# Kernel tuning notes

Measured on AMD Instinct MI355X. Metric: run time of the kernel, lower is better.

The kernel has to match this reference:

```python
import jax, jax.numpy as jnp
import numpy as np

N_NODES = 50000
N_EDGES = 1200000
H = 64
N_CONV = 3
N_GRAPHS = 64
N_CLASSES = 10


def rbf_cutoff(d):
    # Gaussian radial basis over (0,1) with cosine cutoff, per edge -> [E, H]
    mu = jnp.linspace(0.0, 1.0, H, dtype=d.dtype)
    gamma = jnp.asarray(float(H), d.dtype)  # inverse width
    bf = jnp.exp(-gamma * (d[:, None] - mu[None, :]) ** 2)
    cut = 0.5 * (jnp.cos(jnp.pi * jnp.clip(d, 0.0, 1.0)) + 1.0)
    return bf * cut[:, None]


def mlp(x, W1, b1, W2, b2):
    # Linear -> softplus -> Linear (SchNet-style filter/embedding MLP)
    return jax.nn.softplus(x @ W1 + b1) @ W2 + b2


def setup_inputs() -> dict:
    key = jax.random.key(0)
    ks = jax.random.split(key, 12)
    s = 0.1  # weight scale for numerical stability
    inp = {
        "d": jax.random.uniform(ks[0], (N_EDGES,), jnp.float32),
        "W_emb1": s * jax.random.normal(ks[1], (H, H), jnp.float32),
        "b_emb1": jnp.zeros((H,), jnp.float32),
        "W_emb2": s * jax.random.normal(ks[2], (H, H), jnp.float32),
        "b_emb2": jnp.zeros((H,), jnp.float32),
        "filt_W1": s * jax.random.normal(ks[3], (N_CONV, H, H), jnp.float32),
        "filt_b1": jnp.zeros((N_CONV, H), jnp.float32),
        "filt_W2": s * jax.random.normal(ks[4], (N_CONV, H, H), jnp.float32),
        "filt_b2": jnp.zeros((N_CONV, H), jnp.float32),
        "W_in": s * jax.random.normal(ks[5], (N_CONV, H, H), jnp.float32),
        "b_in": jnp.zeros((N_CONV, H), jnp.float32),
        "W_out": s * jax.random.normal(ks[6], (N_CONV, H, H), jnp.float32),
        "b_out": jnp.zeros((N_CONV, H), jnp.float32),
        "W_fc": s * jax.random.normal(ks[7], (H, N_CLASSES), jnp.float32),
        "b_fc": jnp.zeros((N_CLASSES,), jnp.float32),
        "src": jax.random.randint(ks[8], (N_EDGES,), 0, N_NODES, jnp.int32),
        "dst": jax.random.randint(ks[9], (N_EDGES,), 0, N_NODES, jnp.int32),
        "node_graph_ids": jnp.sort(jax.random.randint(ks[10], (N_NODES,), 0, N_GRAPHS, jnp.int32)),
    }
    return inp


def reference(d, W_emb1, b_emb1, W_emb2, b_emb2,
              filt_W1, filt_b1, filt_W2, filt_b2,
              W_in, b_in, W_out, b_out, W_fc, b_fc,
              src, dst, node_graph_ids):
    bf = rbf_cutoff(d)  # [E, H], basis * cutoff (g.edata['bf'])

    # SchnetEmbedding: MLP over radial features, scatter-add to destination nodes
    x = jax.ops.segment_sum(mlp(bf, W_emb1, b_emb1, W_emb2, b_emb2),
                            dst, num_segments=N_NODES)  # [N, H]

    # Stacked SchnetConv: gather x[src] -> in-proj -> radial filter modulation -> scatter-add -> out-proj
    for l in range(N_CONV):
        filt = mlp(bf, filt_W1[l], filt_b1[l], filt_W2[l], filt_b2[l])  # [E, H]
        m = (x[src] @ W_in[l] + b_in[l]) * filt                          # [E, H]
        agg = jax.ops.segment_sum(m, dst, num_segments=N_NODES)         # [N, H]
        x = jax.nn.relu(agg @ W_out[l] + b_out[l])

    # dgl.mean_nodes: per-graph mean pooling
    counts = jax.ops.segment_sum(jnp.ones((N_NODES,), x.dtype),
                                 node_graph_ids, num_segments=N_GRAPHS)
    pooled = jax.ops.segment_sum(x, node_graph_ids, num_segments=N_GRAPHS)
    pooled = pooled / jnp.maximum(counts, 1.0)[:, None]  # [B, H]

    logits = pooled @ W_fc + b_fc
    return jax.nn.log_softmax(logits, axis=1)
```

## Files before the change

kernel.cpp:

```cpp
#include <hip/hip_runtime.h>
#include <math.h>

#define H 64
#define NCONV 3
#define NGRAPHS 64
#define NCLASSES 10
#define TBL 8192
#define TROWS (TBL + 1)

typedef unsigned short bfu;

__device__ __forceinline__ float bf2f(bfu u) {
    return __uint_as_float(((unsigned int)u) << 16);
}
__device__ __forceinline__ bfu f2bf(float f) {
    unsigned int x = __float_as_uint(f);
    return (bfu)((x + 0x7FFF + ((x >> 16) & 1)) >> 16);
}
__device__ __forceinline__ float softplus_f(float x) {
    return fmaxf(x, 0.f) + log1pf(expf(-fabsf(x)));
}
__device__ __forceinline__ float bflo(unsigned int u) { return __uint_as_float(u << 16); }
__device__ __forceinline__ float bfhi(unsigned int u) { return __uint_as_float(u & 0xFFFF0000u); }

__device__ __forceinline__ unsigned int ld_rec_nt(const unsigned int* p) {
    return __builtin_nontemporal_load(p);
}
#define REC_SRC(u) ((u) & 0x1FFFFu)
#define REC_T(u)   ((u) >> 17)

__global__ void build_tables(const float* __restrict__ W_emb1, const float* __restrict__ b_emb1,
                             const float* __restrict__ W_emb2, const float* __restrict__ b_emb2,
                             const float* __restrict__ fW1, const float* __restrict__ fb1,
                             const float* __restrict__ fW2, const float* __restrict__ fb2,
                             bfu* __restrict__ tabs)
{
    int which = blockIdx.y;
    const float *W1, *b1, *W2, *b2;
    if (which == 0) { W1 = W_emb1; b1 = b_emb1; W2 = W_emb2; b2 = b_emb2; }
    else {
        int l = which - 1;
        W1 = fW1 + l * H * H; b1 = fb1 + l * H;
        W2 = fW2 + l * H * H; b2 = fb2 + l * H;
    }

    __shared__ float sW1[H * H], sW2[H * H];
    __shared__ float sb1[H], sb2[H];
    __shared__ float sha[4][H], shb[4][H];

    int tid = threadIdx.x;
    for (int i = tid; i < H * H; i += 256) { sW1[i] = W1[i]; sW2[i] = W2[i]; }
    if (tid < H) sb1[tid] = b1[tid];
    else if (tid < 2 * H) sb2[tid - H] = b2[tid - H];
    __syncthreads();

    int wave = tid >> 6, lane = tid & 63;
    int base = blockIdx.x * 64;
    int lim  = min(base + 64, TROWS);

    for (int r = base + wave; r < lim; r += 4) {
        float dv   = (float)r / (float)TBL;
        float mu   = (float)lane / (float)(H - 1);
        float diff = dv - mu;
        float cut  = 0.5f * (cosf(3.14159265358979323846f * dv) + 1.0f);
        float bfj  = expf(-(float)H * diff * diff) * cut;

        sha[wave][lane] = bfj;
        float a = sb1[lane];
        #pragma unroll
        for (int i = 0; i < H; ++i) a = fmaf(sha[wave][i], sW1[i * H + lane], a);
        shb[wave][lane] = softplus_f(a);
        float a2 = sb2[lane];
        #pragma unroll
        for (int i = 0; i < H; ++i) a2 = fmaf(shb[wave][i], sW2[i * H + lane], a2);

        tabs[((size_t)which * TROWS + r) * H + lane] = f2bf(a2);
    }
}

__global__ void hist_rank(const int* __restrict__ dst, int* __restrict__ cnt,
                          int* __restrict__ rank, int E) {
    int e = blockIdx.x * blockDim.x + threadIdx.x;
    if (e < E) rank[e] = atomicAdd(&cnt[dst[e]], 1);
}

__global__ void scan_bsum(const int* __restrict__ cnt, int* __restrict__ bsum, int N) {
    __shared__ int s[256];
    int t = threadIdx.x;
    int i = blockIdx.x * 256 + t;
    s[t] = (i < N) ? cnt[i] : 0;
    __syncthreads();
    for (int o = 128; o > 0; o >>= 1) {
        if (t < o) s[t] += s[t + o];
        __syncthreads();
    }
    if (t == 0) bsum[blockIdx.x] = s[0];
}

__global__ void scan_gsum(const int* __restrict__ bsum, int* __restrict__ gsum, int nblk) {
    __shared__ int s[1024];
    int t = threadIdx.x;
    s[t] = (t < nblk) ? bsum[t] : 0;
    __syncthreads();
    for (int o = 1; o < 1024; o <<= 1) {
        int v = (t >= o) ? s[t - o] : 0;
        __syncthreads();
        s[t] += v;
        __syncthreads();
    }
    if (t < nblk) gsum[t] = s[t] - bsum[t];
}

__global__ void scan_off(const int* __restrict__ cnt, const int* __restrict__ gsum,
                         int* __restrict__ off, int N) {
    __shared__ int s[256];
    int t = threadIdx.x;
    int i = blockIdx.x * 256 + t;
    int v = (i < N) ? cnt[i] : 0;
    s[t] = v;
    __syncthreads();
    for (int o = 1; o < 256; o <<= 1) {
        int u = (t >= o) ? s[t - o] : 0;
        __syncthreads();
        s[t] += u;
        __syncthreads();
    }
    int incl = s[t] + gsum[blockIdx.x];
    if (i < N) {
        off[i] = incl - v;
        if (i == N - 1) off[N] = incl;
    }
}

__global__ void scatter_kernel(const int* __restrict__ src, const int* __restrict__ dst,
                               const float* __restrict__ d, const int* __restrict__ off,
                               const int* __restrict__ rank, unsigned int* __restrict__ recs, int E)
{
    int e = blockIdx.x * blockDim.x + threadIdx.x;
    if (e >= E) return;
    int pos = off[dst[e]] + rank[e];
    float dv = fminf(fmaxf(d[e], 0.f), 1.f);
    int t = (int)(dv * (float)TBL + 0.5f);
    t = min(t, TBL);
    recs[pos] = (unsigned int)src[e] | ((unsigned int)t << 17);
}

__global__ void emb_fused(const int* __restrict__ off, const unsigned int* __restrict__ recs,
                          const bfu* __restrict__ tab, const float* __restrict__ W,
                          const float* __restrict__ bvec, bfu* __restrict__ yout, int N)
{
    __shared__ float sW[H * H];
    __shared__ float sb[H];
    __shared__ float sx[4][H];
    int tid = threadIdx.x;
    for (int i = tid; i < H * H; i += 256) sW[i] = W[i];
    if (tid < H) sb[tid] = bvec[tid];
    __syncthreads();

    const unsigned int* tab32 = (const unsigned int*)tab;

    int wave = tid >> 6, lane = tid & 63;
    int half = lane >> 5;
    int li   = lane & 31;

    for (int k = 0; k < 4; ++k) {
        int node = blockIdx.x * 16 + k * 4 + wave;
        if (node >= N) continue;
        int b = off[node], en = off[node + 1];
        int deg = en - b;
        int c0  = (deg + 1) >> 1;
        int p   = b + half * c0;
        int e   = (half == 0) ? (b + c0) : en;

        float a0 = 0.f, a1 = 0.f, a2 = 0.f, a3 = 0.f;

        if (e - p >= 8) {
            unsigned int u0 = ld_rec_nt(recs + p);
            unsigned int u1 = ld_rec_nt(recs + p + 1);
            unsigned int u2 = ld_rec_nt(recs + p + 2);
            unsigned int u3 = ld_rec_nt(recs + p + 3);
            unsigned int tv0 = tab32[(size_t)REC_T(u0) * 32 + li];
            unsigned int tv1 = tab32[(size_t)REC_T(u1) * 32 + li];
            unsigned int tv2 = tab32[(size_t)REC_T(u2) * 32 + li];
            unsigned int tv3 = tab32[(size_t)REC_T(u3) * 32 + li];
            u0 = ld_rec_nt(recs + p + 4);
            u1 = ld_rec_nt(recs + p + 5);
            u2 = ld_rec_nt(recs + p + 6);
            u3 = ld_rec_nt(recs + p + 7);
            while (p + 12 <= e) {
                unsigned int w0 = ld_rec_nt(recs + p + 8);
                unsigned int w1 = ld_rec_nt(recs + p + 9);
                unsigned int w2 = ld_rec_nt(recs + p + 10);
                unsigned int w3 = ld_rec_nt(recs + p + 11);
                unsigned int n0 = tab32[(size_t)REC_T(u0) * 32 + li];
                unsigned int n1 = tab32[(size_t)REC_T(u1) * 32 + li];
                unsigned int n2 = tab32[(size_t)REC_T(u2) * 32 + li];
                unsigned int n3 = tab32[(size_t)REC_T(u3) * 32 + li];
                a0 += bflo(tv0); a1 += bfhi(tv0);
                a2 += bflo(tv1); a3 += bfhi(tv1);
                a0 += bflo(tv2); a1 += bfhi(tv2);
                a2 += bflo(tv3); a3 += bfhi(tv3);
                tv0 = n0; tv1 = n1; tv2 = n2; tv3 = n3;
                u0 = w0; u1 = w1; u2 = w2; u3 = w3;
                p += 4;
            }
            unsigned int n0 = tab32[(size_t)REC_T(u0) * 32 + li];
            unsigned int n1 = tab32[(size_t)REC_T(u1) * 32 + li];
            unsigned int n2 = tab32[(size_t)REC_T(u2) * 32 + li];
            unsigned int n3 = tab32[(size_t)REC_T(u3) * 32 + li];
            a0 += bflo(tv0); a1 += bfhi(tv0);
            a2 += bflo(tv1); a3 += bfhi(tv1);
            a0 += bflo(tv2); a1 += bfhi(tv2);
            a2 += bflo(tv3); a3 += bfhi(tv3);
            a0 += bflo(n0); a1 += bfhi(n0);
            a2 += bflo(n1); a3 += bfhi(n1);
            a0 += bflo(n2); a1 += bfhi(n2);
            a2 += bflo(n3); a3 += bfhi(n3);
            p += 8;
        } else if (e - p >= 4) {
            unsigned int u0 = ld_rec_nt(recs + p);
            unsigned int u1 = ld_rec_nt(recs + p + 1);
            unsigned int u2 = ld_rec_nt(recs + p + 2);
            unsigned int u3 = ld_rec_nt(recs + p + 3);
            unsigned int n0 = tab32[(size_t)REC_T(u0) * 32 + li];
            unsigned int n1 = tab32[(size_t)REC_T(u1) * 32 + li];
            unsigned int n2 = tab32[(size_t)REC_T(u2) * 32 + li];
            unsigned int n3 = tab32[(size_t)REC_T(u3) * 32 + li];
            a0 += bflo(n0); a1 += bfhi(n0);
            a2 += bflo(n1); a3 += bfhi(n1);
            a0 += bflo(n2); a1 += bfhi(n2);
            a2 += bflo(n3); a3 += bfhi(n3);
            p += 4;
        }
        for (; p < e; ++p) {
            unsigned int u = ld_rec_nt(recs + p);
            unsigned int t = tab32[(size_t)REC_T(u) * 32 + li];
            a0 += bflo(t); a1 += bfhi(t);
        }

        float alo = a0 + a2, ahi = a1 + a3;
        alo += __shfl_down(alo, 32);
        ahi += __shfl_down(ahi, 32);
        if (lane < 32) {
            sx[wave][2 * li]     = alo;
            sx[wave][2 * li + 1] = ahi;
        }
        float o = sb[lane];
        #pragma unroll
        for (int i = 0; i < H; ++i) o = fmaf(sx[wave][i], sW[i * H + lane], o);
        yout[(size_t)node * H + lane] = f2bf(o);
    }
}

template <bool LAST>
__global__ void conv_fused_k(const int* __restrict__ off, const unsigned int* __restrict__ recs,
                             const bfu* __restrict__ tab, const bfu* __restrict__ y,
                             const float* __restrict__ W_out, const float* __restrict__ b_out,
                             bfu* __restrict__ yout, float* __restrict__ xout, int N)
{
    __shared__ float sW[H * H];
    __shared__ float sb[H];
    __shared__ float sx[4][H];
    int tid = threadIdx.x;
    for (int i = tid; i < H * H; i += 256) sW[i] = W_out[i];
    if (tid < H) sb[tid] = b_out[tid];
    __syncthreads();

    const unsigned int* tab32 = (const unsigned int*)tab;
    const unsigned int* y32   = (const unsigned int*)y;

    int wave = tid >> 6, lane = tid & 63;
    int half = lane >> 5;
    int li   = lane & 31;

    for (int k = 0; k < 4; ++k) {
        int node = blockIdx.x * 16 + k * 4 + wave;
        if (node >= N) continue;
        int b = off[node], en = off[node + 1];
        int deg = en - b;
        int c0  = (deg + 1) >> 1;
        int p   = b + half * c0;
        int e   = (half == 0) ? (b + c0) : en;

        float a0 = 0.f, a1 = 0.f, a2 = 0.f, a3 = 0.f;

        if (e - p >= 8) {
            unsigned int u0 = ld_rec_nt(recs + p);
            unsigned int u1 = ld_rec_nt(recs + p + 1);
            unsigned int u2 = ld_rec_nt(recs + p + 2);
            unsigned int u3 = ld_rec_nt(recs + p + 3);
            unsigned int tv0 = tab32[(size_t)REC_T(u0) * 32 + li];
            unsigned int yv0 = y32[(size_t)REC_SRC(u0) * 32 + li];
            unsigned int tv1 = tab32[(size_t)REC_T(u1) * 32 + li];
            unsigned int yv1 = y32[(size_t)REC_SRC(u1) * 32 + li];
            unsigned int tv2 = tab32[(size_t)REC_T(u2) * 32 + li];
            unsigned int yv2 = y32[(size_t)REC_SRC(u2) * 32 + li];
            unsigned int tv3 = tab32[(size_t)REC_T(u3) * 32 + li];
            unsigned int yv3 = y32[(size_t)REC_SRC(u3) * 32 + li];
            u0 = ld_rec_nt(recs + p + 4);
            u1 = ld_rec_nt(recs + p + 5);
            u2 = ld_rec_nt(recs + p + 6);
            u3 = ld_rec_nt(recs + p + 7);
            while (p + 12 <= e) {
                unsigned int w0 = ld_rec_nt(recs + p + 8);
                unsigned int w1 = ld_rec_nt(recs + p + 9);
                unsigned int w2 = ld_rec_nt(recs + p + 10);
                unsigned int w3 = ld_rec_nt(recs + p + 11);
                unsigned int nt0 = tab32[(size_t)REC_T(u0) * 32 + li];
                unsigned int ny0 = y32[(size_t)REC_SRC(u0) * 32 + li];
                unsigned int nt1 = tab32[(size_t)REC_T(u1) * 32 + li];
                unsigned int ny1 = y32[(size_t)REC_SRC(u1) * 32 + li];
                unsigned int nt2 = tab32[(size_t)REC_T(u2) * 32 + li];
                unsigned int ny2 = y32[(size_t)REC_SRC(u2) * 32 + li];
                unsigned int nt3 = tab32[(size_t)REC_T(u3) * 32 + li];
                unsigned int ny3 = y32[(size_t)REC_SRC(u3) * 32 + li];
                a0 = fmaf(bflo(yv0), bflo(tv0), a0);
                a1 = fmaf(bfhi(yv0), bfhi(tv0), a1);
                a2 = fmaf(bflo(yv1), bflo(tv1), a2);
                a3 = fmaf(bfhi(yv1), bfhi(tv1), a3);
                a0 = fmaf(bflo(yv2), bflo(tv2), a0);
                a1 = fmaf(bfhi(yv2), bfhi(tv2), a1);
                a2 = fmaf(bflo(yv3), bflo(tv3), a2);
                a3 = fmaf(bfhi(yv3), bfhi(tv3), a3);
                tv0 = nt0; yv0 = ny0; tv1 = nt1; yv1 = ny1;
                tv2 = nt2; yv2 = ny2; tv3 = nt3; yv3 = ny3;
                u0 = w0; u1 = w1; u2 = w2; u3 = w3;
                p += 4;
            }
            unsigned int nt0 = tab32[(size_t)REC_T(u0) * 32 + li];
            unsigned int ny0 = y32[(size_t)REC_SRC(u0) * 32 + li];
            unsigned int nt1 = tab32[(size_t)REC_T(u1) * 32 + li];
            unsigned int ny1 = y32[(size_t)REC_SRC(u1) * 32 + li];
            unsigned int nt2 = tab32[(size_t)REC_T(u2) * 32 + li];
            unsigned int ny2 = y32[(size_t)REC_SRC(u2) * 32 + li];
            unsigned int nt3 = tab32[(size_t)REC_T(u3) * 32 + li];
            unsigned int ny3 = y32[(size_t)REC_SRC(u3) * 32 + li];
            a0 = fmaf(bflo(yv0), bflo(tv0), a0);
            a1 = fmaf(bfhi(yv0), bfhi(tv0), a1);
            a2 = fmaf(bflo(yv1), bflo(tv1), a2);
            a3 = fmaf(bfhi(yv1), bfhi(tv1), a3);
            a0 = fmaf(bflo(yv2), bflo(tv2), a0);
            a1 = fmaf(bfhi(yv2), bfhi(tv2), a1);
            a2 = fmaf(bflo(yv3), bflo(tv3), a2);
            a3 = fmaf(bfhi(yv3), bfhi(tv3), a3);
            a0 = fmaf(bflo(ny0), bflo(nt0), a0);
            a1 = fmaf(bfhi(ny0), bfhi(nt0), a1);
            a2 = fmaf(bflo(ny1), bflo(nt1), a2);
            a3 = fmaf(bfhi(ny1), bfhi(nt1), a3);
            a0 = fmaf(bflo(ny2), bflo(nt2), a0);
            a1 = fmaf(bfhi(ny2), bfhi(nt2), a1);
            a2 = fmaf(bflo(ny3), bflo(nt3), a2);
            a3 = fmaf(bfhi(ny3), bfhi(nt3), a3);
            p += 8;
        } else if (e - p >= 4) {
            unsigned int u0 = ld_rec_nt(recs + p);
            unsigned int u1 = ld_rec_nt(recs + p + 1);
            unsigned int u2 = ld_rec_nt(recs + p + 2);
            unsigned int u3 = ld_rec_nt(recs + p + 3);
            unsigned int nt0 = tab32[(size_t)REC_T(u0) * 32 + li];
            unsigned int ny0 = y32[(size_t)REC_SRC(u0) * 32 + li];
            unsigned int nt1 = tab32[(size_t)REC_T(u1) * 32 + li];
            unsigned int ny1 = y32[(size_t)REC_SRC(u1) * 32 + li];
            unsigned int nt2 = tab32[(size_t)REC_T(u2) * 32 + li];
            unsigned int ny2 = y32[(size_t)REC_SRC(u2) * 32 + li];
            unsigned int nt3 = tab32[(size_t)REC_T(u3) * 32 + li];
            unsigned int ny3 = y32[(size_t)REC_SRC(u3) * 32 + li];
            a0 = fmaf(bflo(ny0), bflo(nt0), a0);
            a1 = fmaf(bfhi(ny0), bfhi(nt0), a1);
            a2 = fmaf(bflo(ny1), bflo(nt1), a2);
            a3 = fmaf(bfhi(ny1), bfhi(nt1), a3);
            a0 = fmaf(bflo(ny2), bflo(nt2), a0);
            a1 = fmaf(bfhi(ny2), bfhi(nt2), a1);
            a2 = fmaf(bflo(ny3), bflo(nt3), a2);
            a3 = fmaf(bfhi(ny3), bfhi(nt3), a3);
            p += 4;
        }
        for (; p < e; ++p) {
            unsigned int u = ld_rec_nt(recs + p);
            unsigned int t = tab32[(size_t)REC_T(u) * 32 + li];
            unsigned int v = y32[(size_t)REC_SRC(u) * 32 + li];
            a0 = fmaf(bflo(v), bflo(t), a0);
            a1 = fmaf(bfhi(v), bfhi(t), a1);
        }

        float alo = a0 + a2, ahi = a1 + a3;
        alo += __shfl_down(alo, 32);
        ahi += __shfl_down(ahi, 32);
        if (lane < 32) {
            sx[wave][2 * li]     = alo;
            sx[wave][2 * li + 1] = ahi;
        }
        float o = sb[lane];
        #pragma unroll
        for (int i = 0; i < H; ++i) o = fmaf(sx[wave][i], sW[i * H + lane], o);
        o = fmaxf(o, 0.f);
        if (LAST) xout[(size_t)node * H + lane] = o;
        else      yout[(size_t)node * H + lane] = f2bf(o);
    }
}

__global__ void node_proj(const bfu* __restrict__ xin, const float* __restrict__ W,
                          const float* __restrict__ bvec, bfu* __restrict__ yout, int N)
{
    __shared__ float sW[H * H];
    __shared__ float sb[H];
    __shared__ float sx[4][H];
    int tid = threadIdx.x;
    for (int i = tid; i < H * H; i += 256) sW[i] = W[i];
    if (tid < H) sb[tid] = bvec[tid];
    __syncthreads();

    int wave = tid >> 6, lane = tid & 63;
    for (int k = 0; k < 4; ++k) {
        int node = blockIdx.x * 16 + k * 4 + wave;
        if (node >= N) continue;
        sx[wave][lane] = bf2f(xin[(size_t)node * H + lane]);
        float o = sb[lane];
        #pragma unroll
        for (int i = 0; i < H; ++i) o = fmaf(sx[wave][i], sW[i * H + lane], o);
        yout[(size_t)node * H + lane] = f2bf(o);
    }
}

__global__ void pool_kernel(const float* __restrict__ x, const int* __restrict__ gid,
                            float* __restrict__ pooled, float* __restrict__ counts, int N)
{
    int wavesPerBlock = blockDim.x >> 6;
    int wid  = blockIdx.x * wavesPerBlock + (threadIdx.x >> 6);
    int lane = threadIdx.x & 63;
    int totalWaves = gridDim.x * wavesPerBlock;
    int chunk = (N + totalWaves - 1) / totalWaves;
    int beg = wid * chunk, end = min(beg + chunk, N);
    if (beg >= end) return;

    float acc = 0.f;
    int cur = -1, cnt = 0;
    for (int n = beg; n < end; ++n) {
        int g = gid[n];
        if (g != cur) {
            if (cur >= 0) {
                atomicAdd(&pooled[(size_t)cur * H + lane], acc);
                if (lane == 0) atomicAdd(&counts[cur], (float)cnt);
            }
            cur = g; acc = 0.f; cnt = 0;
        }
        acc += x[(size_t)n * H + lane];
        cnt++;
    }
    atomicAdd(&pooled[(size_t)cur * H + lane], acc);
    if (lane == 0) atomicAdd(&counts[cur], (float)cnt);
}

__global__ void head_kernel(const float* __restrict__ pooled, const float* __restrict__ counts,
                            const float* __restrict__ Wfc, const float* __restrict__ bfc,
                            float* __restrict__ out)
{
    int g = blockIdx.x;
    int c = threadIdx.x;
    __shared__ float logits[NCLASSES];
    float cnt = fmaxf(counts[g], 1.0f);
    if (c < NCLASSES) {
        float acc = bfc[c];
        #pragma unroll
        for (int i = 0; i < H; ++i)
            acc = fmaf(pooled[(size_t)g * H + i] / cnt, Wfc[i * NCLASSES + c], acc);
        logits[c] = acc;
    }
    __syncthreads();
    if (c < NCLASSES) {
        float m = -INFINITY;
        #pragma unroll
        for (int k = 0; k < NCLASSES; ++k) m = fmaxf(m, logits[k]);
        float s = 0.f;
        #pragma unroll
        for (int k = 0; k < NCLASSES; ++k) s += expf(logits[k] - m);
        out[g * NCLASSES + c] = logits[c] - m - logf(s);
    }
}

extern "C" void kernel_launch(void* const* d_in, const int* in_sizes, int n_in,
                              void* d_out, int out_size, void* d_ws, size_t ws_size,
                              hipStream_t stream)
{
    const float* d_d    = (const float*)d_in[0];
    const float* W_emb1 = (const float*)d_in[1];
    const float* b_emb1 = (const float*)d_in[2];
    const float* W_emb2 = (const float*)d_in[3];
    const float* b_emb2 = (const float*)d_in[4];
    const float* fW1    = (const float*)d_in[5];
    const float* fb1    = (const float*)d_in[6];
    const float* fW2    = (const float*)d_in[7];
    const float* fb2    = (const float*)d_in[8];
    const float* W_in   = (const float*)d_in[9];
    const float* b_in   = (const float*)d_in[10];
    const float* W_out  = (const float*)d_in[11];
    const float* b_out  = (const float*)d_in[12];
    const float* W_fc   = (const float*)d_in[13];
    const float* b_fc   = (const float*)d_in[14];
    const int*   src    = (const int*)d_in[15];
    const int*   dst    = (const int*)d_in[16];
    const int*   gid    = (const int*)d_in[17];

    const int E = in_sizes[0];
    const int N = in_sizes[17];

    float* out = (float*)d_out;

    char* base = (char*)d_ws;
    unsigned int* recs = (unsigned int*)base;   base += (size_t)E * 4;
    int*  rank   = (int*)base;                  base += (size_t)E * 4;
    bfu*  tabs   = (bfu*)base;                  base += (size_t)4 * TROWS * H * 2;
    bfu*  yA     = (bfu*)base;                  base += (size_t)N * H * 2;
    bfu*  xB     = (bfu*)base;                  base += (size_t)N * H * 2;
    float* x3    = (float*)base;                base += (size_t)N * H * 4;
    float* pooled= (float*)base;                base += (size_t)NGRAPHS * H * 4;
    float* counts= (float*)base;                base += (size_t)NGRAPHS * 4;
    int*  cnt    = (int*)base;                  base += (size_t)N * 4;
    int*  off    = (int*)base;                  base += (size_t)(N + 1) * 4;
    int*  bsum   = (int*)base;                  base += (size_t)1024 * 4;
    int*  gsum   = (int*)base;                  base += (size_t)1024 * 4;

    const int edge_tblocks  = (E + 255) / 256;
    const int node_blocks16 = (N + 15) / 16;
    const int scan_blocks   = (N + 255) / 256;

    dim3 tg((TROWS + 63) / 64, 4);
    build_tables<<<tg, 256, 0, stream>>>(W_emb1, b_emb1, W_emb2, b_emb2,
                                         fW1, fb1, fW2, fb2, tabs);

    hipMemsetAsync(cnt, 0, (size_t)N * 4, stream);
    hist_rank<<<edge_tblocks, 256, 0, stream>>>(dst, cnt, rank, E);
    scan_bsum<<<scan_blocks, 256, 0, stream>>>(cnt, bsum, N);
    scan_gsum<<<1, 1024, 0, stream>>>(bsum, gsum, scan_blocks);
    scan_off<<<scan_blocks, 256, 0, stream>>>(cnt, gsum, off, N);
    scatter_kernel<<<edge_tblocks, 256, 0, stream>>>(src, dst, d_d, off, rank, recs, E);

    emb_fused<<<node_blocks16, 256, 0, stream>>>(off, recs, tabs, W_in, b_in, yA, N);

    conv_fused_k<false><<<node_blocks16, 256, 0, stream>>>(
        off, recs, tabs + (size_t)1 * TROWS * H, yA, W_out, b_out, xB, nullptr, N);
    node_proj<<<node_blocks16, 256, 0, stream>>>(
        xB, W_in + (size_t)1 * H * H, b_in + (size_t)1 * H, yA, N);

    conv_fused_k<false><<<node_blocks16, 256, 0, stream>>>(
        off, recs, tabs + (size_t)2 * TROWS * H, yA,
        W_out + (size_t)1 * H * H, b_out + (size_t)1 * H, xB, nullptr, N);
    node_proj<<<node_blocks16, 256, 0, stream>>>(
        xB, W_in + (size_t)2 * H * H, b_in + (size_t)2 * H, yA, N);

    conv_fused_k<true><<<node_blocks16, 256, 0, stream>>>(
        off, recs, tabs + (size_t)3 * TROWS * H, yA,
        W_out + (size_t)2 * H * H, b_out + (size_t)2 * H, nullptr, x3, N);

    hipMemsetAsync(pooled, 0, ((size_t)NGRAPHS * H + NGRAPHS) * 4, stream);
    pool_kernel<<<128, 256, 0, stream>>>(x3, gid, pooled, counts, N);

    head_kernel<<<NGRAPHS, 64, 0, stream>>>(pooled, counts, W_fc, b_fc, out);
}
```

Before: 392.7 us.

## Replace atomic CSR build with two-level bucket sort and fuse node projection into conv

Replaces the global-atomic histogram, three-pass scan and scatter that built the destination-sorted edge list with a two-level partition. A coarse pass bins edges by dst>>8 using shared-memory atomics into fixed-capacity buckets, and a per-bucket fine sort builds the offsets and the final records. The separate node_proj kernel is folded into the conv kernel epilogue, with both weight matrices stored in shared memory as packed bf16. This removes the rank array, several launches and one node-feature round trip, but a fixed bucket capacity (CAP) can overflow if degrees cluster, and the bf16 weights reduce precision.

```diff
diff --git a/kernel.cpp b/kernel.cpp
--- a/kernel.cpp
+++ b/kernel.cpp
@@ -7,6 +7,8 @@
 #define NCLASSES 10
 #define TBL 8192
 #define TROWS (TBL + 1)
+#define CAP 6144
+#define EPT 8
 
 typedef unsigned short bfu;
 
@@ -78,45 +80,58 @@
     }
 }
 
-__global__ void hist_rank(const int* __restrict__ dst, int* __restrict__ cnt,
-                          int* __restrict__ rank, int E) {
-    int e = blockIdx.x * blockDim.x + threadIdx.x;
-    if (e < E) rank[e] = atomicAdd(&cnt[dst[e]], 1);
-}
-
-__global__ void scan_bsum(const int* __restrict__ cnt, int* __restrict__ bsum, int N) {
+__global__ void coarse_part(const int* __restrict__ src, const int* __restrict__ dst,
+                            const float* __restrict__ d, int* __restrict__ ccur,
+                            unsigned long long* __restrict__ cbuf, int E, int ncb)
+{
+    __shared__ int lcnt[256];
+    __shared__ int lbase[256];
+    int tid = threadIdx.x;
+    int e0  = blockIdx.x * (256 * EPT);
+
+    lcnt[tid] = 0;
+    __syncthreads();
+
+    int mybin[EPT], myrank[EPT];
+    unsigned long long myrec[EPT];
+    #pragma unroll
+    for (int k = 0; k < EPT; ++k) {
+        int e = e0 + k * 256 + tid;
+        mybin[k] = -1;
+        if (e < E) {
+            int v = dst[e];
+            int bin = v >> 8;
+            float dv = fminf(fmaxf(d[e], 0.f), 1.f);
+            int t = (int)(dv * (float)TBL + 0.5f);
+            t = min(t, TBL);
+            unsigned int p31 = (unsigned int)src[e] | ((unsigned int)t << 17);
+            myrec[k]  = (unsigned long long)p31 | ((unsigned long long)(v & 255) << 32);
+            mybin[k]  = bin;
+            myrank[k] = atomicAdd(&lcnt[bin], 1);
+        }
+    }
+    __syncthreads();
+
+    {
+        int c = (tid < ncb) ? lcnt[tid] : 0;
+        lbase[tid] = (c > 0) ? atomicAdd(&ccur[tid], c) : 0;
+    }
+    __syncthreads();
+
+    #pragma unroll
+    for (int k = 0; k < EPT; ++k) {
+        if (mybin[k] >= 0) {
+            cbuf[(size_t)mybin[k] * CAP + lbase[mybin[k]] + myrank[k]] = myrec[k];
+        }
+    }
+}
+
+__global__ void cscan(const int* __restrict__ ccur, int* __restrict__ cstart,
+                      int* __restrict__ off, int E, int N, int ncb)
+{
     __shared__ int s[256];
     int t = threadIdx.x;
-    int i = blockIdx.x * 256 + t;
-    s[t] = (i < N) ? cnt[i] : 0;
-    __syncthreads();
-    for (int o = 128; o > 0; o >>= 1) {
-        if (t < o) s[t] += s[t + o];
-        __syncthreads();
-    }
-    if (t == 0) bsum[blockIdx.x] = s[0];
-}
-
-__global__ void scan_gsum(const int* __restrict__ bsum, int* __restrict__ gsum, int nblk) {
-    __shared__ int s[1024];
-    int t = threadIdx.x;
-    s[t] = (t < nblk) ? bsum[t] : 0;
-    __syncthreads();
-    for (int o = 1; o < 1024; o <<= 1) {
-        int v = (t >= o) ? s[t - o] : 0;
-        __syncthreads();
-        s[t] += v;
-        __syncthreads();
-    }
-    if (t < nblk) gsum[t] = s[t] - bsum[t];
-}
-
-__global__ void scan_off(const int* __restrict__ cnt, const int* __restrict__ gsum,
-                         int* __restrict__ off, int N) {
-    __shared__ int s[256];
-    int t = threadIdx.x;
-    int i = blockIdx.x * 256 + t;
-    int v = (i < N) ? cnt[i] : 0;
+    int v = (t < ncb) ? ccur[t] : 0;
     s[t] = v;
     __syncthreads();
     for (int o = 1; o < 256; o <<= 1) {
@@ -125,24 +140,50 @@
         s[t] += u;
         __syncthreads();
     }
-    int incl = s[t] + gsum[blockIdx.x];
-    if (i < N) {
-        off[i] = incl - v;
-        if (i == N - 1) off[N] = incl;
-    }
-}
-
-__global__ void scatter_kernel(const int* __restrict__ src, const int* __restrict__ dst,
-                               const float* __restrict__ d, const int* __restrict__ off,
-                               const int* __restrict__ rank, unsigned int* __restrict__ recs, int E)
-{
-    int e = blockIdx.x * blockDim.x + threadIdx.x;
-    if (e >= E) return;
-    int pos = off[dst[e]] + rank[e];
-    float dv = fminf(fmaxf(d[e], 0.f), 1.f);
-    int t = (int)(dv * (float)TBL + 0.5f);
-    t = min(t, TBL);
-    recs[pos] = (unsigned int)src[e] | ((unsigned int)t << 17);
+    if (t < ncb) cstart[t] = s[t] - v;
+    if (t == 0) off[N] = E;
+}
+
+__global__ void fine_sort(const unsigned long long* __restrict__ cbuf,
+                          const int* __restrict__ ccur, const int* __restrict__ cstart,
+                          int* __restrict__ off, unsigned int* __restrict__ recs, int N)
+{
+    __shared__ int lcnt[256];
+    __shared__ int ss[256];
+    __shared__ int lcur[256];
+    int bin  = blockIdx.x;
+    int tid  = threadIdx.x;
+    int cnt  = ccur[bin];
+    int base = cstart[bin];
+    const unsigned long long* buf = cbuf + (size_t)bin * CAP;
+
+    lcnt[tid] = 0;
+    __syncthreads();
+    for (int i = tid; i < cnt; i += 256) {
+        int j = (int)((buf[i] >> 32) & 255);
+        atomicAdd(&lcnt[j], 1);
+    }
+    __syncthreads();
+    int v = lcnt[tid];
+    ss[tid] = v;
+    __syncthreads();
+    for (int o = 1; o < 256; o <<= 1) {
+        int u = (tid >= o) ? ss[tid - o] : 0;
+        __syncthreads();
+        ss[tid] += u;
+        __syncthreads();
+    }
+    int excl = ss[tid] - v;
+    lcur[tid] = excl;
+    int node = bin * 256 + tid;
+    if (node < N) off[node] = base + excl;
+    __syncthreads();
+    for (int i = tid; i < cnt; i += 256) {
+        unsigned long long r = buf[i];
+        int j = (int)((r >> 32) & 255);
+        int pos = base + atomicAdd(&lcur[j], 1);
+        recs[pos] = (unsigned int)(r & 0x7FFFFFFFu);
+    }
 }
 
 __global__ void emb_fused(const int* __restrict__ off, const unsigned int* __restrict__ recs,
@@ -256,14 +297,24 @@
 __global__ void conv_fused_k(const int* __restrict__ off, const unsigned int* __restrict__ recs,
                              const bfu* __restrict__ tab, const bfu* __restrict__ y,
                              const float* __restrict__ W_out, const float* __restrict__ b_out,
+                             const float* __restrict__ W_in, const float* __restrict__ b_in,
                              bfu* __restrict__ yout, float* __restrict__ xout, int N)
 {
-    __shared__ float sW[H * H];
-    __shared__ float sb[H];
+    __shared__ unsigned int sWo[H * H / 2];
+    __shared__ unsigned int sWi[H * H / 2];
+    __shared__ float sbo[H], sbi[H];
     __shared__ float sx[4][H];
     int tid = threadIdx.x;
-    for (int i = tid; i < H * H; i += 256) sW[i] = W_out[i];
-    if (tid < H) sb[tid] = b_out[tid];
+    for (int i = tid; i < H * H / 2; i += 256) {
+        int i2 = i >> 6, l = i & 63;
+        sWo[i] = (unsigned int)f2bf(W_out[(2 * i2) * H + l]) |
+                 ((unsigned int)f2bf(W_out[(2 * i2 + 1) * H + l]) << 16);
+        if (!LAST)
+            sWi[i] = (unsigned int)f2bf(W_in[(2 * i2) * H + l]) |
+                     ((unsigned int)f2bf(W_in[(2 * i2 + 1) * H + l]) << 16);
+    }
+    if (tid < H) sbo[tid] = b_out[tid];
+    else if (!LAST && tid < 2 * H) sbi[tid - H] = b_in[tid - H];
     __syncthreads();
 
     const unsigned int* tab32 = (const unsigned int*)tab;
@@ -390,35 +441,27 @@
             sx[wave][2 * li]     = alo;
             sx[wave][2 * li + 1] = ahi;
         }
-        float o = sb[lane];
-        #pragma unroll
-        for (int i = 0; i < H; ++i) o = fmaf(sx[wave][i], sW[i * H + lane], o);
+        float o = sbo[lane];
+        #pragma unroll
+        for (int i2 = 0; i2 < H / 2; ++i2) {
+            unsigned int u = sWo[i2 * H + lane];
+            o = fmaf(sx[wave][2 * i2],     bflo(u), o);
+            o = fmaf(sx[wave][2 * i2 + 1], bfhi(u), o);
+        }
         o = fmaxf(o, 0.f);
-        if (LAST) xout[(size_t)node * H + lane] = o;
-        else      yout[(size_t)node * H + lane] = f2bf(o);
-    }
-}
-
-__global__ void node_proj(const bfu* __restrict__ xin, const float* __restrict__ W,
-                          const float* __restrict__ bvec, bfu* __restrict__ yout, int N)
-{
-    __shared__ float sW[H * H];
-    __shared__ float sb[H];
-    __shared__ float sx[4][H];
-    int tid = threadIdx.x;
-    for (int i = tid; i < H * H; i += 256) sW[i] = W[i];
-    if (tid < H) sb[tid] = bvec[tid];
-    __syncthreads();
-
-    int wave = tid >> 6, lane = tid & 63;
-    for (int k = 0; k < 4; ++k) {
-        int node = blockIdx.x * 16 + k * 4 + wave;
-        if (node >= N) continue;
-        sx[wave][lane] = bf2f(xin[(size_t)node * H + lane]);
-        float o = sb[lane];
-        #pragma unroll
-        for (int i = 0; i < H; ++i) o = fmaf(sx[wave][i], sW[i * H + lane], o);
-        yout[(size_t)node * H + lane] = f2bf(o);
+        if (LAST) {
+            xout[(size_t)node * H + lane] = o;
+        } else {
+            sx[wave][lane] = o;
+            float o2 = sbi[lane];
+            #pragma unroll
+            for (int i2 = 0; i2 < H / 2; ++i2) {
+                unsigned int u = sWi[i2 * H + lane];
+                o2 = fmaf(sx[wave][2 * i2],     bflo(u), o2);
+                o2 = fmaf(sx[wave][2 * i2 + 1], bfhi(u), o2);
+            }
+            yout[(size_t)node * H + lane] = f2bf(o2);
+        }
     }
 }
 
@@ -503,54 +546,51 @@
 
     const int E = in_sizes[0];
     const int N = in_sizes[17];
+    const int ncb = (N + 255) >> 8;
 
     float* out = (float*)d_out;
 
     char* base = (char*)d_ws;
     unsigned int* recs = (unsigned int*)base;   base += (size_t)E * 4;
-    int*  rank   = (int*)base;                  base += (size_t)E * 4;
     bfu*  tabs   = (bfu*)base;                  base += (size_t)4 * TROWS * H * 2;
     bfu*  yA     = (bfu*)base;                  base += (size_t)N * H * 2;
-    bfu*  xB     = (bfu*)base;                  base += (size_t)N * H * 2;
-    float* x3    = (float*)base;                base += (size_t)N * H * 4;
+    bfu*  yB     = (bfu*)base;                  base += (size_t)N * H * 2;
+    size_t usz   = (size_t)N * H * 4;
+    size_t csz   = (size_t)ncb * CAP * 8;
+    char* uni    = base;                        base += (usz > csz ? usz : csz);
+    float* x3    = (float*)uni;
+    unsigned long long* cbuf = (unsigned long long*)uni;
     float* pooled= (float*)base;                base += (size_t)NGRAPHS * H * 4;
     float* counts= (float*)base;                base += (size_t)NGRAPHS * 4;
-    int*  cnt    = (int*)base;                  base += (size_t)N * 4;
     int*  off    = (int*)base;                  base += (size_t)(N + 1) * 4;
-    int*  bsum   = (int*)base;                  base += (size_t)1024 * 4;
-    int*  gsum   = (int*)base;                  base += (size_t)1024 * 4;
-
-    const int edge_tblocks  = (E + 255) / 256;
+    int*  ccur   = (int*)base;                  base += 256 * 4;
+    int*  cstart = (int*)base;                  base += 256 * 4;
+
     const int node_blocks16 = (N + 15) / 16;
-    const int scan_blocks   = (N + 255) / 256;
+    const int part_blocks   = (E + 256 * EPT - 1) / (256 * EPT);
 
     dim3 tg((TROWS + 63) / 64, 4);
     build_tables<<<tg, 256, 0, stream>>>(W_emb1, b_emb1, W_emb2, b_emb2,
                                          fW1, fb1, fW2, fb2, tabs);
 
-    hipMemsetAsync(cnt, 0, (size_t)N * 4, stream);
-    hist_rank<<<edge_tblocks, 256, 0, stream>>>(dst, cnt, rank, E);
-    scan_bsum<<<scan_blocks, 256, 0, stream>>>(cnt, bsum, N);
-    scan_gsum<<<1, 1024, 0, stream>>>(bsum, gsum, scan_blocks);
-    scan_off<<<scan_blocks, 256, 0, stream>>>(cnt, gsum, off, N);
-    scatter_kernel<<<edge_tblocks, 256, 0, stream>>>(src, dst, d_d, off, rank, recs, E);
+    hipMemsetAsync(ccur, 0, 256 * 4, stream);
+    coarse_part<<<part_blocks, 256, 0, stream>>>(src, dst, d_d, ccur, cbuf, E, ncb);
+    cscan<<<1, 256, 0, stream>>>(ccur, cstart, off, E, N, ncb);
+    fine_sort<<<ncb, 256, 0, stream>>>(cbuf, ccur, cstart, off, recs, N);
 
     emb_fused<<<node_blocks16, 256, 0, stream>>>(off, recs, tabs, W_in, b_in, yA, N);
 
     conv_fused_k<false><<<node_blocks16, 256, 0, stream>>>(
-        off, recs, tabs + (size_t)1 * TROWS * H, yA, W_out, b_out, xB, nullptr, N);
-    node_proj<<<node_blocks16, 256, 0, stream>>>(
-        xB, W_in + (size_t)1 * H * H, b_in + (size_t)1 * H, yA, N);
-
+        off, recs, tabs + (size_t)1 * TROWS * H, yA,
+        W_out, b_out, W_in + (size_t)1 * H * H, b_in + (size_t)1 * H, yB, nullptr, N);
     conv_fused_k<false><<<node_blocks16, 256, 0, stream>>>(
-        off, recs, tabs + (size_t)2 * TROWS * H, yA,
-        W_out + (size_t)1 * H * H, b_out + (size_t)1 * H, xB, nullptr, N);
-    node_proj<<<node_blocks16, 256, 0, stream>>>(
-        xB, W_in + (size_t)2 * H * H, b_in + (size_t)2 * H, yA, N);
-
+        off, recs, tabs + (size_t)2 * TROWS * H, yB,
+        W_out + (size_t)1 * H * H, b_out + (size_t)1 * H,
+        W_in + (size_t)2 * H * H, b_in + (size_t)2 * H, yA, nullptr, N);
     conv_fused_k<true><<<node_blocks16, 256, 0, stream>>>(
         off, recs, tabs + (size_t)3 * TROWS * H, yA,
-        W_out + (size_t)2 * H * H, b_out + (size_t)2 * H, nullptr, x3, N);
+        W_out + (size_t)2 * H * H, b_out + (size_t)2 * H,
+        nullptr, nullptr, nullptr, x3, N);
 
     hipMemsetAsync(pooled, 0, ((size_t)NGRAPHS * H + NGRAPHS) * 4, stream);
     pool_kernel<<<128, 256, 0, stream>>>(x3, gid, pooled, counts, N);
```

New measurement: 321.6 us. -18.1%, faster.
